# Kernel optimization log

Hardware: AMD Instinct MI355X
Metric: run time of the kernel (lower is better)

## Reference

```python
import jax, jax.numpy as jnp
import numpy as np

B, G, D, H, W = 2, 8, 32, 128, 160
NEIGH = 9           # evaluate_neighbors
PROP = 1            # propagation_out_range - 1
PAD1 = int(np.sqrt(NEIGH) / 2) + PROP      # = 2
PAD2 = PAD1 * 2                            # = 4


def setup_inputs() -> dict:
    key = jax.random.key(0)
    ks = jax.random.split(key, 8)
    x1 = jax.random.normal(ks[0], (B, G, D, H, W), jnp.float32)
    offset = jax.random.uniform(ks[1], (B, 2 * NEIGH, H, W), jnp.float32)
    weight = jax.random.uniform(ks[2], (B, 1, H, W), jnp.float32)
    # 1x1x1 Conv3d weights stored as [out_ch, in_ch]; BN folded to scale/bias (eval mode)
    w0 = jax.random.normal(ks[3], (16, G), jnp.float32) * 0.1
    bn0_scale = jnp.ones((16,), jnp.float32)
    bn0_bias = jnp.zeros((16,), jnp.float32)
    w1 = jax.random.normal(ks[4], (8, 16), jnp.float32) * 0.1
    bn1_scale = jnp.ones((8,), jnp.float32)
    bn1_bias = jnp.zeros((8,), jnp.float32)
    w_sim = jax.random.normal(ks[5], (1, 8), jnp.float32) * 0.1
    b_sim = jnp.zeros((1,), jnp.float32)
    return {"x1": x1, "offset": offset, "weight": weight,
            "w0": w0, "bn0_scale": bn0_scale, "bn0_bias": bn0_bias,
            "w1": w1, "bn1_scale": bn1_scale, "bn1_bias": bn1_bias,
            "w_sim": w_sim, "b_sim": b_sim}


def _conv1x1_bn_relu(x, w, scale, bias):
    # x: [B,Cin,D,H,W], w: [Cout,Cin]
    y = jnp.einsum('bcdhw,oc->bodhw', x, w)
    return jax.nn.relu(y * scale[None, :, None, None, None] + bias[None, :, None, None, None])


def reference(x1, offset, weight, w0, bn0_scale, bn0_bias, w1, bn1_scale, bn1_bias, w_sim, b_sim):
    h = _conv1x1_bn_relu(x1, w0, bn0_scale, bn0_bias)          # [B,16,D,H,W]
    h = _conv1x1_bn_relu(h, w1, bn1_scale, bn1_bias)            # [B,8,D,H,W]
    sim = jnp.einsum('bcdhw,oc->bodhw', h, w_sim) + b_sim[None, :, None, None, None]
    sim = sim[:, 0]                                             # [B,D,H,W]
    b, d, hgt, wid = sim.shape
    p1 = jnp.pad(sim, ((0, 0), (0, 0), (PAD1, PAD1), (PAD1, PAD1)), mode='reflect')
    p2 = jnp.pad(sim, ((0, 0), (0, 0), (PAD2, PAD2), (PAD2, PAD2)), mode='reflect')
    side = int(np.sqrt(NEIGH))  # 3
    acc = jnp.zeros_like(sim)
    for s in range(NEIGH):
        iy, ix = s // side, s % side
        # wide-dilation crop (stride (PROP+1)*2 = 4) over the double-padded map
        c2 = p2[:, :, iy * 4: iy * 4 + hgt, ix * 4: ix * 4 + wid]
        # narrow-dilation crop (stride PROP+1 = 2) over the single-padded map
        c1 = p1[:, :, iy * 2: iy * 2 + hgt, ix * 2: ix * 2 + wid]
        w_wide = offset[:, s][:, None]            # [B,1,H,W] -> broadcast over depth
        w_narrow = offset[:, s + NEIGH][:, None]
        acc = acc + (w_narrow * c1 + w_wide * c2) * 0.5
    return acc * weight                                          # weight [B,1,H,W]
```

## Files before the change

### kernel.cpp

```cpp
#include <hip/hip_runtime.h>

#define Bc 2
#define Gc 8
#define Dc 32
#define Hc 128
#define Wc 160
#define HW (Hc * Wc)
#define DHW (Dc * HW)

__global__ __launch_bounds__(256) void mlp_kernel(
    const float* __restrict__ x1,
    const float* __restrict__ w0, const float* __restrict__ s0, const float* __restrict__ b0,
    const float* __restrict__ w1, const float* __restrict__ s1, const float* __restrict__ b1,
    const float* __restrict__ wsim, const float* __restrict__ bsim,
    float* __restrict__ sim)
{
    __shared__ float smw[289];
    const int tid = threadIdx.x;
    for (int i = tid; i < 289; i += 256) {
        float v;
        if (i < 128)      v = w0[i] * s0[i >> 3];
        else if (i < 144) v = b0[i - 128];
        else if (i < 272) v = w1[i - 144] * s1[(i - 144) >> 4];
        else if (i < 280) v = b1[i - 272];
        else if (i < 288) v = wsim[i - 280];
        else              v = bsim[0];
        smw[i] = v;
    }
    __syncthreads();
    const float* sw0 = smw;
    const float* sb0 = smw + 128;
    const float* sw1 = smw + 144;
    const float* sb1 = smw + 272;
    const float* sws = smw + 280;
    const float  sbs = smw[288];

    const int t   = blockIdx.x * 256 + tid;
    const int p   = t << 2;
    const int b   = p / DHW;
    const int dhw = p - b * DHW;
    const float* xb = x1 + (size_t)b * (Gc * DHW) + dhw;

    float4 xv[Gc];
#pragma unroll
    for (int g = 0; g < Gc; ++g)
        xv[g] = *reinterpret_cast<const float4*>(xb + g * DHW);

    float4 acc1[8];
#pragma unroll
    for (int c = 0; c < 8; ++c) {
        const float bb = sb1[c];
        acc1[c].x = bb; acc1[c].y = bb; acc1[c].z = bb; acc1[c].w = bb;
    }

#pragma unroll
    for (int o = 0; o < 16; ++o) {
        float ax = sb0[o], ay = ax, az = ax, aw = ax;
#pragma unroll
        for (int g = 0; g < Gc; ++g) {
            const float wv = sw0[o * Gc + g];
            ax = fmaf(wv, xv[g].x, ax);
            ay = fmaf(wv, xv[g].y, ay);
            az = fmaf(wv, xv[g].z, az);
            aw = fmaf(wv, xv[g].w, aw);
        }
        ax = fmaxf(ax, 0.f);
        ay = fmaxf(ay, 0.f);
        az = fmaxf(az, 0.f);
        aw = fmaxf(aw, 0.f);
#pragma unroll
        for (int c = 0; c < 8; ++c) {
            const float wv = sw1[c * 16 + o];
            acc1[c].x = fmaf(wv, ax, acc1[c].x);
            acc1[c].y = fmaf(wv, ay, acc1[c].y);
            acc1[c].z = fmaf(wv, az, acc1[c].z);
            acc1[c].w = fmaf(wv, aw, acc1[c].w);
        }
    }

    float sx = sbs, sy = sbs, sz = sbs, sw = sbs;
#pragma unroll
    for (int c = 0; c < 8; ++c) {
        const float ws = sws[c];
        sx = fmaf(ws, fmaxf(acc1[c].x, 0.f), sx);
        sy = fmaf(ws, fmaxf(acc1[c].y, 0.f), sy);
        sz = fmaf(ws, fmaxf(acc1[c].z, 0.f), sz);
        sw = fmaf(ws, fmaxf(acc1[c].w, 0.f), sw);
    }

    float4 r; r.x = sx; r.y = sy; r.z = sz; r.w = sw;
    *reinterpret_cast<float4*>(sim + p) = r;
}

__global__ __launch_bounds__(256) void agg_kernel(
    const float* __restrict__ sim, const float* __restrict__ offset,
    const float* __restrict__ weight, float* __restrict__ out)
{
    const int l  = blockIdx.x * 256 + threadIdx.x;
    const int q  = l % (Wc / 4);
    const int w4 = q * 4;
    int r = l / (Wc / 4);
    const int h = r % Hc;
    r /= Hc;
    const int d = r & 31;
    const int b = r >> 5;
    const int hw4 = h * Wc + w4;

    const float* offb = offset + (size_t)b * 18 * HW;
    float4 off4[18];
#pragma unroll
    for (int s = 0; s < 18; ++s)
        off4[s] = *reinterpret_cast<const float4*>(offb + s * HW + hw4);
    float4 wt4 = *reinterpret_cast<const float4*>(weight + (size_t)b * HW + hw4);
    wt4.x *= 0.5f; wt4.y *= 0.5f; wt4.z *= 0.5f; wt4.w *= 0.5f;

    int y1[3], y2[3];
#pragma unroll
    for (int iy = 0; iy < 3; ++iy) {
        int a1 = h + (iy - 1) * 2; y1[iy] = a1 < 0 ? -a1 : (a1 >= Hc ? 2 * Hc - 2 - a1 : a1);
        int a2 = h + (iy - 1) * 4; y2[iy] = a2 < 0 ? -a2 : (a2 >= Hc ? 2 * Hc - 2 - a2 : a2);
    }

    const float* sp = sim + (size_t)(b * Dc + d) * HW;
    float ax = 0.f, ay = 0.f, az = 0.f, aw = 0.f;

    if (w4 >= 4 && w4 <= Wc - 8) {
#pragma unroll
        for (int s = 0; s < 9; ++s) {
            const int iy = s / 3, ix = s % 3;
            const float4 cw = *reinterpret_cast<const float4*>(
                sp + y2[iy] * Wc + w4 + (ix - 1) * 4);
            const float* np = sp + y1[iy] * Wc + w4 + (ix - 1) * 2;
            const float2 n0 = *reinterpret_cast<const float2*>(np);
            const float2 n1 = *reinterpret_cast<const float2*>(np + 2);
            const float4 ow = off4[s];
            const float4 on = off4[s + 9];
            ax = fmaf(on.x, n0.x, fmaf(ow.x, cw.x, ax));
            ay = fmaf(on.y, n0.y, fmaf(ow.y, cw.y, ay));
            az = fmaf(on.z, n1.x, fmaf(ow.z, cw.z, az));
            aw = fmaf(on.w, n1.y, fmaf(ow.w, cw.w, aw));
        }
    } else {
        float acc[4] = {0.f, 0.f, 0.f, 0.f};
#pragma unroll
        for (int j = 0; j < 4; ++j) {
            const int w = w4 + j;
            float a = 0.f;
#pragma unroll
            for (int s = 0; s < 9; ++s) {
                const int iy = s / 3, ix = s % 3;
                int x1c = w + (ix - 1) * 2; x1c = x1c < 0 ? -x1c : (x1c >= Wc ? 2 * Wc - 2 - x1c : x1c);
                int x2c = w + (ix - 1) * 4; x2c = x2c < 0 ? -x2c : (x2c >= Wc ? 2 * Wc - 2 - x2c : x2c);
                const float on = j == 0 ? off4[s + 9].x : j == 1 ? off4[s + 9].y : j == 2 ? off4[s + 9].z : off4[s + 9].w;
                const float ow = j == 0 ? off4[s].x     : j == 1 ? off4[s].y     : j == 2 ? off4[s].z     : off4[s].w;
                a = fmaf(on, sp[y1[iy] * Wc + x1c], fmaf(ow, sp[y2[iy] * Wc + x2c], a));
            }
            acc[j] = a;
        }
        ax = acc[0]; ay = acc[1]; az = acc[2]; aw = acc[3];
    }

    float4 o4;
    o4.x = ax * wt4.x;
    o4.y = ay * wt4.y;
    o4.z = az * wt4.z;
    o4.w = aw * wt4.w;
    float* outb = out + (size_t)(b * Dc + d) * HW;
    *reinterpret_cast<float4*>(outb + hw4) = o4;
}

extern "C" void kernel_launch(void* const* d_in, const int* in_sizes, int n_in,
                              void* d_out, int out_size, void* d_ws, size_t ws_size,
                              hipStream_t stream)
{
    const float* x1     = (const float*)d_in[0];
    const float* offset = (const float*)d_in[1];
    const float* weight = (const float*)d_in[2];
    const float* w0     = (const float*)d_in[3];
    const float* s0     = (const float*)d_in[4];
    const float* b0     = (const float*)d_in[5];
    const float* w1     = (const float*)d_in[6];
    const float* s1     = (const float*)d_in[7];
    const float* b1     = (const float*)d_in[8];
    const float* wsim   = (const float*)d_in[9];
    const float* bsim   = (const float*)d_in[10];
    float* out = (float*)d_out;
    float* sim = (float*)d_ws;

    mlp_kernel<<<1280, 256, 0, stream>>>(x1, w0, s0, b0, w1, s1, b1, wsim, bsim, sim);
    agg_kernel<<<1280, 256, 0, stream>>>(sim, offset, weight, out);
}
```

Measured before the change: 115.4 us.

## Fuse MLP and aggregation into one cooperative kernel with grid sync

Merges the two kernel launches into a single cooperative launch that computes the similarity map, runs a grid-wide barrier, and then does the neighbor aggregation in the same blocks. The aim is to drop the second launch and the gap between kernels. It needs all 1280 blocks to be resident at once, so it checks occupancy (at least 5 blocks per CU) and falls back to two launches if that fails. The grid barrier costs time, and because both phases now share one kernel, register pressure and occupancy may change.

```diff
diff --git a/kernel.cpp b/kernel.cpp
--- a/kernel.cpp
+++ b/kernel.cpp
@@ -1,22 +1,23 @@
 #include <hip/hip_runtime.h>
-
-#define Bc 2
+#include <hip/hip_cooperative_groups.h>
+
+namespace cg = cooperative_groups;
+
 #define Gc 8
 #define Dc 32
 #define Hc 128
 #define Wc 160
 #define HW (Hc * Wc)
 #define DHW (Dc * HW)
-
-__global__ __launch_bounds__(256) void mlp_kernel(
-    const float* __restrict__ x1,
-    const float* __restrict__ w0, const float* __restrict__ s0, const float* __restrict__ b0,
-    const float* __restrict__ w1, const float* __restrict__ s1, const float* __restrict__ b1,
-    const float* __restrict__ wsim, const float* __restrict__ bsim,
-    float* __restrict__ sim)
-{
-    __shared__ float smw[289];
-    const int tid = threadIdx.x;
+#define NTHREADS 327680
+#define NBLOCKS 1280
+
+__device__ __forceinline__ void stage_weights(
+    float* smw, int tid,
+    const float* w0, const float* s0, const float* b0,
+    const float* w1, const float* s1, const float* b1,
+    const float* wsim, const float* bsim)
+{
     for (int i = tid; i < 289; i += 256) {
         float v;
         if (i < 128)      v = w0[i] * s0[i >> 3];
@@ -27,7 +28,12 @@
         else              v = bsim[0];
         smw[i] = v;
     }
-    __syncthreads();
+}
+
+__device__ __forceinline__ void mlp_body(
+    int t, const float* __restrict__ x1, const float* smw,
+    float* __restrict__ sim)
+{
     const float* sw0 = smw;
     const float* sb0 = smw + 128;
     const float* sw1 = smw + 144;
@@ -35,7 +41,6 @@
     const float* sws = smw + 280;
     const float  sbs = smw[288];
 
-    const int t   = blockIdx.x * 256 + tid;
     const int p   = t << 2;
     const int b   = p / DHW;
     const int dhw = p - b * DHW;
@@ -92,11 +97,10 @@
     *reinterpret_cast<float4*>(sim + p) = r;
 }
 
-__global__ __launch_bounds__(256) void agg_kernel(
-    const float* __restrict__ sim, const float* __restrict__ offset,
+__device__ __forceinline__ void agg_body(
+    int l, const float* __restrict__ sim, const float* __restrict__ offset,
     const float* __restrict__ weight, float* __restrict__ out)
 {
-    const int l  = blockIdx.x * 256 + threadIdx.x;
     const int q  = l % (Wc / 4);
     const int w4 = q * 4;
     int r = l / (Wc / 4);
@@ -169,6 +173,45 @@
     *reinterpret_cast<float4*>(outb + hw4) = o4;
 }
 
+__global__ __launch_bounds__(256) void fused_coop(
+    const float* __restrict__ x1, const float* __restrict__ offset,
+    const float* __restrict__ weight,
+    const float* __restrict__ w0, const float* __restrict__ s0, const float* __restrict__ b0,
+    const float* __restrict__ w1, const float* __restrict__ s1, const float* __restrict__ b1,
+    const float* __restrict__ wsim, const float* __restrict__ bsim,
+    float* __restrict__ sim, float* __restrict__ out)
+{
+    __shared__ float smw[289];
+    const int tid = threadIdx.x;
+    stage_weights(smw, tid, w0, s0, b0, w1, s1, b1, wsim, bsim);
+    __syncthreads();
+    const int t = blockIdx.x * 256 + tid;
+    mlp_body(t, x1, smw, sim);
+    cg::this_grid().sync();
+    agg_body(t, sim, offset, weight, out);
+}
+
+__global__ __launch_bounds__(256) void mlp_kernel(
+    const float* __restrict__ x1,
+    const float* __restrict__ w0, const float* __restrict__ s0, const float* __restrict__ b0,
+    const float* __restrict__ w1, const float* __restrict__ s1, const float* __restrict__ b1,
+    const float* __restrict__ wsim, const float* __restrict__ bsim,
+    float* __restrict__ sim)
+{
+    __shared__ float smw[289];
+    const int tid = threadIdx.x;
+    stage_weights(smw, tid, w0, s0, b0, w1, s1, b1, wsim, bsim);
+    __syncthreads();
+    mlp_body(blockIdx.x * 256 + tid, x1, smw, sim);
+}
+
+__global__ __launch_bounds__(256) void agg_kernel(
+    const float* __restrict__ sim, const float* __restrict__ offset,
+    const float* __restrict__ weight, float* __restrict__ out)
+{
+    agg_body(blockIdx.x * 256 + threadIdx.x, sim, offset, weight, out);
+}
+
 extern "C" void kernel_launch(void* const* d_in, const int* in_sizes, int n_in,
                               void* d_out, int out_size, void* d_ws, size_t ws_size,
                               hipStream_t stream)
@@ -187,6 +230,25 @@
     float* out = (float*)d_out;
     float* sim = (float*)d_ws;
 
-    mlp_kernel<<<1280, 256, 0, stream>>>(x1, w0, s0, b0, w1, s1, b1, wsim, bsim, sim);
-    agg_kernel<<<1280, 256, 0, stream>>>(sim, offset, weight, out);
-}
+    static int coop_ok = -1;
+    if (coop_ok < 0) {
+        int maxb = 0;
+        hipError_t e = hipOccupancyMaxActiveBlocksPerMultiprocessor(
+            &maxb, fused_coop, 256, 0);
+        coop_ok = (e == hipSuccess && maxb >= 5) ? 1 : 0;
+    }
+
+    if (coop_ok) {
+        void* args[] = { (void*)&x1, (void*)&offset, (void*)&weight,
+                         (void*)&w0, (void*)&s0, (void*)&b0,
+                         (void*)&w1, (void*)&s1, (void*)&b1,
+                         (void*)&wsim, (void*)&bsim,
+                         (void*)&sim, (void*)&out };
+        hipLaunchCooperativeKernel((const void*)fused_coop,
+                                   dim3(NBLOCKS), dim3(256), args, 0, stream);
+    } else {
+        mlp_kernel<<<NBLOCKS, 256, 0, stream>>>(x1, w0, s0, b0, w1, s1, b1,
+                                                wsim, bsim, sim);
+        agg_kernel<<<NBLOCKS, 256, 0, stream>>>(sim, offset, weight, out);
+    }
+}
```

New measurement: 115.6 us. Within noise of the previous version (+0.2%).
